# Performance work log

Measured on AMD Instinct MI355X. Metric: run time of the kernel, lower is better.

Reference implementation:

```python
import jax, jax.numpy as jnp
import numpy as np

KB = 0.0019872041      # Boltzmann constant, kcal/(mol*K)
TEMP = 300.0
ALPHA = 10.0
BW = 0.15              # Gaussian KDE bandwidth
PAIR_I = jnp.array([0, 0, 0, 1, 1, 2])
PAIR_J = jnp.array([1, 2, 3, 2, 3, 3])

B, N_ATOMS = 512, 1024
G, L, K, D = 256, 8, 128, 6


def setup_inputs() -> dict:
    key = jax.random.key(0)
    k1, k2, k3, k4, k5, k6 = jax.random.split(key, 6)
    positions = jax.random.normal(k1, (B, N_ATOMS, 3), dtype=jnp.float32) * 2.0
    # KDE training samples live in 6-dim distance space (positive, few Angstroms)
    kde_samples = jax.random.uniform(k2, (G, L, K, D), dtype=jnp.float32) * 5.0
    weight = jax.random.uniform(k3, (G, L), dtype=jnp.float32)
    offset = jax.random.normal(k4, (G, L), dtype=jnp.float32)
    atom_idxs = jax.random.randint(k5, (G, L, 4), 0, N_ATOMS)
    group_sizes = jax.random.randint(k6, (G,), 0, L)  # clamped to >=1 in reference
    return {"positions": positions, "kde_samples": kde_samples, "weight": weight,
            "offset": offset, "atom_idxs": atom_idxs, "group_sizes": group_sizes}


def reference(positions, kde_samples, weight, offset, atom_idxs, group_sizes):
    Gn, Ln, Kn, Dn = kde_samples.shape
    # Gather the 4 vertices of every loss: [B, G, L, 4, 3]
    vp = positions[:, atom_idxs]
    # 6 pairwise distances per loss: [B, G, L, 6]
    diff = vp[..., PAIR_I, :] - vp[..., PAIR_J, :]
    dists = jnp.sqrt(jnp.sum(diff * diff, axis=-1) + 1e-12)
    # Gaussian KDE log-density over the K training samples, expanded squared
    x2 = jnp.sum(dists * dists, axis=-1)          # [B,G,L]
    mu2 = jnp.sum(kde_samples * kde_samples, -1)  # [G,L,K]
    xmu = jnp.einsum('bgld,glkd->bglk', dists, kde_samples)
    sq = x2[..., None] + mu2[None] - 2.0 * xmu    # [B,G,L,K]
    log_norm = jnp.log(jnp.float32(Kn)) + 0.5 * Dn * jnp.log(2.0 * jnp.pi * BW * BW)
    logP = jax.nn.logsumexp(-sq / (2.0 * BW * BW), axis=-1) - log_norm  # [B,G,L]
    energy = -KB * TEMP * logP
    scaled = energy * weight + offset             # [B,G,L]
    # Ragged group reduction: min over the valid losses of each group
    sizes = jnp.maximum(group_sizes, 1)
    mask = jnp.arange(Ln)[None, :] < sizes[:, None]        # [G,L]
    group_min = jnp.min(jnp.where(mask, scaled, jnp.inf), axis=-1)  # [B,G]
    # soft-min across groups
    return -jax.nn.logsumexp(-ALPHA * group_min, axis=-1) / ALPHA   # [B]
```

## Files before the change

kernel.cpp:

```cpp
#include <hip/hip_runtime.h>

#define NB 512
#define NATOMS 1024
#define NG 256
#define NL 8
#define NK 128

#define KBT 0.59616123f
#define ALPHA_C 10.0f
#define LN2 0.6931471805599453f
#define LOG2E 1.4426950408889634f
#define INV2BW2 22.222221f
#define SCALE2 (INV2BW2 * LOG2E)
#define LOG_NORM (-1.0170649f)

#define WL_CAP 2048
#define FILL_BLOCKS 128

typedef _Float16 f16x8 __attribute__((ext_vector_type(8)));
typedef float f32x16 __attribute__((ext_vector_type(16)));

__device__ __forceinline__ float fexp2(float x) { return __builtin_amdgcn_exp2f(x); }
__device__ __forceinline__ float flog2(float x) { return __builtin_amdgcn_logf(x); }

__device__ __forceinline__ unsigned fkey(float f) {
  unsigned u = __float_as_uint(f);
  return (u & 0x80000000u) ? ~u : (u | 0x80000000u);
}
__device__ __forceinline__ float funkey(unsigned k) {
  unsigned u = (k & 0x80000000u) ? (k ^ 0x80000000u) : ~k;
  return __uint_as_float(u);
}

__device__ __forceinline__ float wred_min(float v) {
#pragma unroll
  for (int m = 32; m >= 1; m >>= 1) v = fminf(v, __shfl_xor(v, m, 64));
  return v;
}
__device__ __forceinline__ float wred_sum(float v) {
#pragma unroll
  for (int m = 32; m >= 1; m >>= 1) v += __shfl_xor(v, m, 64);
  return v;
}

__global__ __launch_bounds__(256) void prep_small(
    const int* __restrict__ gsizes, int* __restrict__ wl,
    uint4* __restrict__ gmin_u4) {
  const int t = threadIdx.x;
  if (blockIdx.x != 0) {
    const unsigned F = 0xFFFFFFFFu;
    gmin_u4[(blockIdx.x - 1) * 256 + t] = make_uint4(F, F, F, F);
    return;
  }
  const int lane = t & 63, wid = t >> 6;
  int gs = gsizes[t];
  int nl = gs < 1 ? 1 : (gs > NL ? NL : gs);
  int x = nl;
#pragma unroll
  for (int m = 1; m < 64; m <<= 1) {
    int y = __shfl_up(x, m, 64);
    if (lane >= m) x += y;
  }
  __shared__ int wsum[4];
  if (lane == 63) wsum[wid] = x;
  __syncthreads();
  int off = 0;
  for (int i = 0; i < wid; ++i) off += wsum[i];
  int inc = off + x, exc = inc - nl;
  for (int j = 0; j < nl; ++j) wl[exc + j] = (t << 3) | j;
  if (t == 255) wl[WL_CAP] = inc;
}

__global__ __launch_bounds__(256) void stage1_kernel(
    const float* __restrict__ positions, const float* __restrict__ kde,
    const float* __restrict__ weight, const float* __restrict__ offs,
    const int* __restrict__ atom_idxs, const int* __restrict__ wl,
    unsigned* __restrict__ gmin_u) {
  const int count = wl[WL_CAP];
  const int w = blockIdx.x >> 2;
  if (w >= count) return;
  const int gl = wl[w];
  const int g = gl >> 3;

  const int t = threadIdx.x;
  const int lane = t & 63;
  const int col = lane & 31, h = lane >> 5;
  const int b = ((blockIdx.x & 3) << 7) + ((t >> 6) << 5) + col;

  __shared__ f16x8 tabL[8][64];

  const int4 idx = *reinterpret_cast<const int4*>(atom_idxs + (gl << 2));
  const int ids[4] = {idx.x, idx.y, idx.z, idx.w};
  const float* pb = positions + (size_t)b * NATOMS * 3;
  float ax[4], ay[4], az[4];
#pragma unroll
  for (int j = 0; j < 4; ++j) {
    const float3 p = *reinterpret_cast<const float3*>(pb + ids[j] * 3);
    ax[j] = p.x; ay[j] = p.y; az[j] = p.z;
  }

  if (t < NK) {
    const float* mp = kde + ((size_t)gl * NK + t) * 6;
    float mu2 = 0.0f;
    _Float16 ah[6], al[6];
#pragma unroll
    for (int q = 0; q < 6; ++q) {
      float mv = mp[q];
      mu2 += mv * mv;
      float a = (2.0f * SCALE2) * mv;
      _Float16 hh = (_Float16)a;
      ah[q] = hh;
      al[q] = (_Float16)(a - (float)hh);
    }
    float z = -SCALE2 * mu2;
    _Float16 z1 = (_Float16)z;
    _Float16 z2 = (_Float16)(z - (float)z1);
    const _Float16 Z = (_Float16)0.0f;
    const int kt = t >> 5, m = t & 31;
    tabL[kt * 2 + 0][m]      = (f16x8){ah[0],ah[1],ah[2],ah[3],ah[4],ah[5],al[0],al[1]};
    tabL[kt * 2 + 0][m + 32] = (f16x8){al[2],al[3],al[4],al[5],ah[0],ah[1],ah[2],ah[3]};
    tabL[kt * 2 + 1][m]      = (f16x8){ah[4],ah[5],al[0],al[1],al[2],al[3],al[4],al[5]};
    tabL[kt * 2 + 1][m + 32] = (f16x8){z1,  z2,  Z,   Z,   Z,   Z,   Z,   Z   };
  }

  const int PI_[6] = {0, 0, 0, 1, 1, 2};
  const int PJ_[6] = {1, 2, 3, 2, 3, 3};
  float d[6]; float x2 = 0.0f;
#pragma unroll
  for (int q = 0; q < 6; ++q) {
    float dx = ax[PI_[q]] - ax[PJ_[q]];
    float dy = ay[PI_[q]] - ay[PJ_[q]];
    float dz = az[PI_[q]] - az[PJ_[q]];
    float dd = dx * dx + dy * dy + dz * dz + 1e-12f;
    d[q] = sqrtf(dd);
    x2 += d[q] * d[q];
  }
  const float c2 = -x2 * SCALE2;

  _Float16 xh[6], xl[6];
#pragma unroll
  for (int q = 0; q < 6; ++q) {
    _Float16 hh = (_Float16)d[q];
    xh[q] = hh;
    xl[q] = (_Float16)(d[q] - (float)hh);
  }
  const _Float16 ONE = (_Float16)1.0f, Z = (_Float16)0.0f;
  f16x8 Bf0 = (h == 0)
    ? (f16x8){xh[0],xh[1],xh[2],xh[3],xh[4],xh[5],xh[0],xh[1]}
    : (f16x8){xh[2],xh[3],xh[4],xh[5],xl[0],xl[1],xl[2],xl[3]};
  f16x8 Bf1 = (h == 0)
    ? (f16x8){xl[4],xl[5],xl[0],xl[1],xl[2],xl[3],xl[4],xl[5]}
    : (f16x8){ONE,  ONE,  Z,   Z,   Z,   Z,   Z,   Z   };

  __syncthreads();

  const f32x16 zz = {0.0f};
  f32x16 acc[4];
#pragma unroll
  for (int kt = 0; kt < 4; ++kt) {
    f16x8 A0 = tabL[kt * 2 + 0][lane];
    f16x8 A1 = tabL[kt * 2 + 1][lane];
    acc[kt] = __builtin_amdgcn_mfma_f32_32x32x16_f16(
        A1, Bf1, __builtin_amdgcn_mfma_f32_32x32x16_f16(A0, Bf0, zz, 0, 0, 0),
        0, 0, 0);
  }

  float mkt[4];
#pragma unroll
  for (int kt = 0; kt < 4; ++kt) {
    float m0 = fmaxf(fmaxf(acc[kt][0], acc[kt][1]), fmaxf(acc[kt][2], acc[kt][3]));
    float m1 = fmaxf(fmaxf(acc[kt][4], acc[kt][5]), fmaxf(acc[kt][6], acc[kt][7]));
    float m2 = fmaxf(fmaxf(acc[kt][8], acc[kt][9]), fmaxf(acc[kt][10], acc[kt][11]));
    float m3 = fmaxf(fmaxf(acc[kt][12], acc[kt][13]), fmaxf(acc[kt][14], acc[kt][15]));
    mkt[kt] = fmaxf(fmaxf(m0, m1), fmaxf(m2, m3));
  }
  float mx = fmaxf(fmaxf(mkt[0], mkt[1]), fmaxf(mkt[2], mkt[3]));
  mx = fmaxf(mx, __shfl_xor(mx, 32, 64));

  float s0 = 0.0f, s1 = 0.0f, s2 = 0.0f, s3 = 0.0f;
#pragma unroll
  for (int kt = 0; kt < 4; ++kt) {
    s0 += fexp2(acc[kt][0] - mx)  + fexp2(acc[kt][1] - mx)
        + fexp2(acc[kt][2] - mx)  + fexp2(acc[kt][3] - mx);
    s1 += fexp2(acc[kt][4] - mx)  + fexp2(acc[kt][5] - mx)
        + fexp2(acc[kt][6] - mx)  + fexp2(acc[kt][7] - mx);
    s2 += fexp2(acc[kt][8] - mx)  + fexp2(acc[kt][9] - mx)
        + fexp2(acc[kt][10] - mx) + fexp2(acc[kt][11] - mx);
    s3 += fexp2(acc[kt][12] - mx) + fexp2(acc[kt][13] - mx)
        + fexp2(acc[kt][14] - mx) + fexp2(acc[kt][15] - mx);
  }
  float s = (s0 + s1) + (s2 + s3);
  s += __shfl_xor(s, 32, 64);

  if (h == 0) {
    float lse2 = c2 + mx + flog2(s);
    float logP = lse2 * LN2 - LOG_NORM;
    float scaled = -KBT * logP * weight[gl] + offs[gl];
    atomicMin(&gmin_u[g * NB + b], fkey(scaled));
  }
}

__global__ __launch_bounds__(256) void stage2_kernel(
    const unsigned* __restrict__ gmin_u, float* __restrict__ out) {
  const int b = blockIdx.x;
  const int t = threadIdx.x;
  const int lane = t & 63;
  const int wid = t >> 6;
  float v = funkey(gmin_u[t * NB + b]);
  __shared__ float sm[4], ss[4];
  float m = wred_min(v);
  if (lane == 0) sm[wid] = m;
  __syncthreads();
  float M = fminf(fminf(sm[0], sm[1]), fminf(sm[2], sm[3]));
  float e = fexp2(-ALPHA_C * LOG2E * (v - M));
  float s = wred_sum(e);
  if (lane == 0) ss[wid] = s;
  __syncthreads();
  if (t == 0) {
    float S = ss[0] + ss[1] + ss[2] + ss[3];
    out[b] = M - flog2(S) * LN2 / ALPHA_C;
  }
}

extern "C" void kernel_launch(void* const* d_in, const int* in_sizes, int n_in,
                              void* d_out, int out_size, void* d_ws, size_t ws_size,
                              hipStream_t stream) {
  const float* positions = (const float*)d_in[0];
  const float* kde       = (const float*)d_in[1];
  const float* weight    = (const float*)d_in[2];
  const float* offs      = (const float*)d_in[3];
  const int*   atom_idxs = (const int*)d_in[4];
  const int*   gsizes    = (const int*)d_in[5];
  float* out = (float*)d_out;

  unsigned* gmin_u = (unsigned*)d_ws;
  int* wl = (int*)d_ws + (size_t)NG * NB;

  prep_small<<<dim3(1 + FILL_BLOCKS), dim3(256), 0, stream>>>(
      gsizes, wl, (uint4*)gmin_u);
  stage1_kernel<<<dim3(WL_CAP * 4), dim3(256), 0, stream>>>(
      positions, kde, weight, offs, atom_idxs, wl, gmin_u);
  stage2_kernel<<<dim3(NB), dim3(256), 0, stream>>>(gmin_u, out);
}
```

Before: 35.85 us.

## Transpose positions to atom-major layout for coalesced gathers in stage1

Adds transpose blocks to the prep kernel that rewrite positions from [B, atoms, 3] into an [atom*3, B] layout in workspace through a shared-memory tile. Stage1 then reads each atom coordinate with consecutive batch indices across lanes, which gives coalesced loads in place of strided 12-byte gathers. The cost is a full read and write of the positions array (about 6 MB each way) in the prep kernel on every call, plus extra workspace.

```diff
diff --git a/kernel.cpp b/kernel.cpp
--- a/kernel.cpp
+++ b/kernel.cpp
@@ -16,6 +16,7 @@
 
 #define WL_CAP 2048
 #define FILL_BLOCKS 128
+#define TR_BLOCKS 256
 
 typedef _Float16 f16x8 __attribute__((ext_vector_type(8)));
 typedef float f32x16 __attribute__((ext_vector_type(16)));
@@ -44,35 +45,67 @@
 }
 
 __global__ __launch_bounds__(256) void prep_small(
-    const int* __restrict__ gsizes, int* __restrict__ wl,
-    uint4* __restrict__ gmin_u4) {
+    const float* __restrict__ positions, const int* __restrict__ gsizes,
+    int* __restrict__ wl, uint4* __restrict__ gmin_u4,
+    float* __restrict__ pT) {
   const int t = threadIdx.x;
-  if (blockIdx.x != 0) {
+  const int bid = blockIdx.x;
+  __shared__ int wsum[4];
+  __shared__ float tile[64][97];
+
+  if (bid == 0) {
+    const int lane = t & 63, wid = t >> 6;
+    int gs = gsizes[t];
+    int nl = gs < 1 ? 1 : (gs > NL ? NL : gs);
+    int x = nl;
+#pragma unroll
+    for (int m = 1; m < 64; m <<= 1) {
+      int y = __shfl_up(x, m, 64);
+      if (lane >= m) x += y;
+    }
+    if (lane == 63) wsum[wid] = x;
+    __syncthreads();
+    int off = 0;
+    for (int i = 0; i < wid; ++i) off += wsum[i];
+    int inc = off + x, exc = inc - nl;
+    for (int j = 0; j < nl; ++j) wl[exc + j] = (t << 3) | j;
+    if (t == 255) wl[WL_CAP] = inc;
+    return;
+  }
+  if (bid <= FILL_BLOCKS) {
     const unsigned F = 0xFFFFFFFFu;
-    gmin_u4[(blockIdx.x - 1) * 256 + t] = make_uint4(F, F, F, F);
+    gmin_u4[(bid - 1) * 256 + t] = make_uint4(F, F, F, F);
     return;
   }
-  const int lane = t & 63, wid = t >> 6;
-  int gs = gsizes[t];
-  int nl = gs < 1 ? 1 : (gs > NL ? NL : gs);
-  int x = nl;
-#pragma unroll
-  for (int m = 1; m < 64; m <<= 1) {
-    int y = __shfl_up(x, m, 64);
-    if (lane >= m) x += y;
-  }
-  __shared__ int wsum[4];
-  if (lane == 63) wsum[wid] = x;
-  __syncthreads();
-  int off = 0;
-  for (int i = 0; i < wid; ++i) off += wsum[i];
-  int inc = off + x, exc = inc - nl;
-  for (int j = 0; j < nl; ++j) wl[exc + j] = (t << 3) | j;
-  if (t == 255) wl[WL_CAP] = inc;
+
+  const int tb = bid - (FILL_BLOCKS + 1);
+  const int a0 = (tb >> 3) << 5;
+  const int b0 = (tb & 7) << 6;
+#pragma unroll
+  for (int iter = 0; iter < 6; ++iter) {
+    const int fi = iter * 256 + t;
+    const int i = fi / 24, s = fi - i * 24;
+    const float4 v = *reinterpret_cast<const float4*>(
+        positions + ((size_t)(b0 + i) * NATOMS + a0) * 3 + s * 4);
+    tile[i][s * 4 + 0] = v.x;
+    tile[i][s * 4 + 1] = v.y;
+    tile[i][s * 4 + 2] = v.z;
+    tile[i][s * 4 + 3] = v.w;
+  }
+  __syncthreads();
+  if (t < 96) {
+    float* dst = pT + ((size_t)a0 * 3 + t) * NB + b0;
+#pragma unroll
+    for (int f = 0; f < 16; ++f) {
+      float4 v = make_float4(tile[4 * f + 0][t], tile[4 * f + 1][t],
+                             tile[4 * f + 2][t], tile[4 * f + 3][t]);
+      *reinterpret_cast<float4*>(dst + 4 * f) = v;
+    }
+  }
 }
 
 __global__ __launch_bounds__(256) void stage1_kernel(
-    const float* __restrict__ positions, const float* __restrict__ kde,
+    const float* __restrict__ pT, const float* __restrict__ kde,
     const float* __restrict__ weight, const float* __restrict__ offs,
     const int* __restrict__ atom_idxs, const int* __restrict__ wl,
     unsigned* __restrict__ gmin_u) {
@@ -91,12 +124,13 @@
 
   const int4 idx = *reinterpret_cast<const int4*>(atom_idxs + (gl << 2));
   const int ids[4] = {idx.x, idx.y, idx.z, idx.w};
-  const float* pb = positions + (size_t)b * NATOMS * 3;
   float ax[4], ay[4], az[4];
 #pragma unroll
   for (int j = 0; j < 4; ++j) {
-    const float3 p = *reinterpret_cast<const float3*>(pb + ids[j] * 3);
-    ax[j] = p.x; ay[j] = p.y; az[j] = p.z;
+    const float* pr = pT + (size_t)ids[j] * 3 * NB + b;
+    ax[j] = pr[0];
+    ay[j] = pr[NB];
+    az[j] = pr[2 * NB];
   }
 
   if (t < NK) {
@@ -235,10 +269,11 @@
 
   unsigned* gmin_u = (unsigned*)d_ws;
   int* wl = (int*)d_ws + (size_t)NG * NB;
-
-  prep_small<<<dim3(1 + FILL_BLOCKS), dim3(256), 0, stream>>>(
-      gsizes, wl, (uint4*)gmin_u);
+  float* pT = (float*)((char*)d_ws + (1 << 20));
+
+  prep_small<<<dim3(1 + FILL_BLOCKS + TR_BLOCKS), dim3(256), 0, stream>>>(
+      positions, gsizes, wl, (uint4*)gmin_u, pT);
   stage1_kernel<<<dim3(WL_CAP * 4), dim3(256), 0, stream>>>(
-      positions, kde, weight, offs, atom_idxs, wl, gmin_u);
+      pT, kde, weight, offs, atom_idxs, wl, gmin_u);
   stage2_kernel<<<dim3(NB), dim3(256), 0, stream>>>(gmin_u, out);
 }
```

After: 38.40 us. 1.07x slower.

## Process all batch chunks per block with double-buffered position prefetch

Applied to the files above, without the earlier changes.

Each stage1 block now handles all four 128-wide batch chunks for one loss instead of one chunk. The KDE table is built in shared memory once and reused four times, which removes three quarters of the table setup and block launches. Position gathers for the next chunk are issued before computing the current one, so their latency overlaps the MFMA and exp work. In exchange there are 4x fewer blocks, which lowers parallelism, and register pressure rises from the double buffer.

```diff
diff --git a/kernel.cpp b/kernel.cpp
--- a/kernel.cpp
+++ b/kernel.cpp
@@ -77,26 +77,30 @@
     const int* __restrict__ atom_idxs, const int* __restrict__ wl,
     unsigned* __restrict__ gmin_u) {
   const int count = wl[WL_CAP];
-  const int w = blockIdx.x >> 2;
+  const int w = blockIdx.x;
   if (w >= count) return;
   const int gl = wl[w];
   const int g = gl >> 3;
 
   const int t = threadIdx.x;
   const int lane = t & 63;
+  const int wid = t >> 6;
   const int col = lane & 31, h = lane >> 5;
-  const int b = ((blockIdx.x & 3) << 7) + ((t >> 6) << 5) + col;
 
   __shared__ f16x8 tabL[8][64];
 
   const int4 idx = *reinterpret_cast<const int4*>(atom_idxs + (gl << 2));
   const int ids[4] = {idx.x, idx.y, idx.z, idx.w};
-  const float* pb = positions + (size_t)b * NATOMS * 3;
-  float ax[4], ay[4], az[4];
-#pragma unroll
-  for (int j = 0; j < 4; ++j) {
-    const float3 p = *reinterpret_cast<const float3*>(pb + ids[j] * 3);
-    ax[j] = p.x; ay[j] = p.y; az[j] = p.z;
+
+  float px[2][4], py[2][4], pz[2][4];
+  {
+    const int b = (wid << 5) + col;
+    const float* pb = positions + (size_t)b * NATOMS * 3;
+#pragma unroll
+    for (int j = 0; j < 4; ++j) {
+      const float3 p = *reinterpret_cast<const float3*>(pb + ids[j] * 3);
+      px[0][j] = p.x; py[0][j] = p.y; pz[0][j] = p.z;
+    }
   }
 
   if (t < NK) {
@@ -122,81 +126,97 @@
     tabL[kt * 2 + 1][m]      = (f16x8){ah[4],ah[5],al[0],al[1],al[2],al[3],al[4],al[5]};
     tabL[kt * 2 + 1][m + 32] = (f16x8){z1,  z2,  Z,   Z,   Z,   Z,   Z,   Z   };
   }
-
+  __syncthreads();
+
+  const float wgt = weight[gl], off = offs[gl];
   const int PI_[6] = {0, 0, 0, 1, 1, 2};
   const int PJ_[6] = {1, 2, 3, 2, 3, 3};
-  float d[6]; float x2 = 0.0f;
-#pragma unroll
-  for (int q = 0; q < 6; ++q) {
-    float dx = ax[PI_[q]] - ax[PJ_[q]];
-    float dy = ay[PI_[q]] - ay[PJ_[q]];
-    float dz = az[PI_[q]] - az[PJ_[q]];
-    float dd = dx * dx + dy * dy + dz * dz + 1e-12f;
-    d[q] = sqrtf(dd);
-    x2 += d[q] * d[q];
-  }
-  const float c2 = -x2 * SCALE2;
-
-  _Float16 xh[6], xl[6];
-#pragma unroll
-  for (int q = 0; q < 6; ++q) {
-    _Float16 hh = (_Float16)d[q];
-    xh[q] = hh;
-    xl[q] = (_Float16)(d[q] - (float)hh);
-  }
   const _Float16 ONE = (_Float16)1.0f, Z = (_Float16)0.0f;
-  f16x8 Bf0 = (h == 0)
-    ? (f16x8){xh[0],xh[1],xh[2],xh[3],xh[4],xh[5],xh[0],xh[1]}
-    : (f16x8){xh[2],xh[3],xh[4],xh[5],xl[0],xl[1],xl[2],xl[3]};
-  f16x8 Bf1 = (h == 0)
-    ? (f16x8){xl[4],xl[5],xl[0],xl[1],xl[2],xl[3],xl[4],xl[5]}
-    : (f16x8){ONE,  ONE,  Z,   Z,   Z,   Z,   Z,   Z   };
-
-  __syncthreads();
-
   const f32x16 zz = {0.0f};
-  f32x16 acc[4];
-#pragma unroll
-  for (int kt = 0; kt < 4; ++kt) {
-    f16x8 A0 = tabL[kt * 2 + 0][lane];
-    f16x8 A1 = tabL[kt * 2 + 1][lane];
-    acc[kt] = __builtin_amdgcn_mfma_f32_32x32x16_f16(
-        A1, Bf1, __builtin_amdgcn_mfma_f32_32x32x16_f16(A0, Bf0, zz, 0, 0, 0),
-        0, 0, 0);
-  }
-
-  float mkt[4];
-#pragma unroll
-  for (int kt = 0; kt < 4; ++kt) {
-    float m0 = fmaxf(fmaxf(acc[kt][0], acc[kt][1]), fmaxf(acc[kt][2], acc[kt][3]));
-    float m1 = fmaxf(fmaxf(acc[kt][4], acc[kt][5]), fmaxf(acc[kt][6], acc[kt][7]));
-    float m2 = fmaxf(fmaxf(acc[kt][8], acc[kt][9]), fmaxf(acc[kt][10], acc[kt][11]));
-    float m3 = fmaxf(fmaxf(acc[kt][12], acc[kt][13]), fmaxf(acc[kt][14], acc[kt][15]));
-    mkt[kt] = fmaxf(fmaxf(m0, m1), fmaxf(m2, m3));
-  }
-  float mx = fmaxf(fmaxf(mkt[0], mkt[1]), fmaxf(mkt[2], mkt[3]));
-  mx = fmaxf(mx, __shfl_xor(mx, 32, 64));
-
-  float s0 = 0.0f, s1 = 0.0f, s2 = 0.0f, s3 = 0.0f;
-#pragma unroll
-  for (int kt = 0; kt < 4; ++kt) {
-    s0 += fexp2(acc[kt][0] - mx)  + fexp2(acc[kt][1] - mx)
-        + fexp2(acc[kt][2] - mx)  + fexp2(acc[kt][3] - mx);
-    s1 += fexp2(acc[kt][4] - mx)  + fexp2(acc[kt][5] - mx)
-        + fexp2(acc[kt][6] - mx)  + fexp2(acc[kt][7] - mx);
-    s2 += fexp2(acc[kt][8] - mx)  + fexp2(acc[kt][9] - mx)
-        + fexp2(acc[kt][10] - mx) + fexp2(acc[kt][11] - mx);
-    s3 += fexp2(acc[kt][12] - mx) + fexp2(acc[kt][13] - mx)
-        + fexp2(acc[kt][14] - mx) + fexp2(acc[kt][15] - mx);
-  }
-  float s = (s0 + s1) + (s2 + s3);
-  s += __shfl_xor(s, 32, 64);
-
-  if (h == 0) {
-    float lse2 = c2 + mx + flog2(s);
-    float logP = lse2 * LN2 - LOG_NORM;
-    float scaled = -KBT * logP * weight[gl] + offs[gl];
-    atomicMin(&gmin_u[g * NB + b], fkey(scaled));
+
+#pragma unroll
+  for (int gg = 0; gg < 4; ++gg) {
+    const int cur = gg & 1;
+    if (gg < 3) {
+      const int bn = ((gg + 1) << 7) + (wid << 5) + col;
+      const float* pb = positions + (size_t)bn * NATOMS * 3;
+#pragma unroll
+      for (int j = 0; j < 4; ++j) {
+        const float3 p = *reinterpret_cast<const float3*>(pb + ids[j] * 3);
+        px[cur ^ 1][j] = p.x; py[cur ^ 1][j] = p.y; pz[cur ^ 1][j] = p.z;
+      }
+    }
+    const int b = (gg << 7) + (wid << 5) + col;
+
+    float d[6]; float x2 = 0.0f;
+#pragma unroll
+    for (int q = 0; q < 6; ++q) {
+      float dx = px[cur][PI_[q]] - px[cur][PJ_[q]];
+      float dy = py[cur][PI_[q]] - py[cur][PJ_[q]];
+      float dz = pz[cur][PI_[q]] - pz[cur][PJ_[q]];
+      float dd = dx * dx + dy * dy + dz * dz + 1e-12f;
+      d[q] = sqrtf(dd);
+      x2 += d[q] * d[q];
+    }
+    const float c2 = -x2 * SCALE2;
+
+    _Float16 xh[6], xl[6];
+#pragma unroll
+    for (int q = 0; q < 6; ++q) {
+      _Float16 hh = (_Float16)d[q];
+      xh[q] = hh;
+      xl[q] = (_Float16)(d[q] - (float)hh);
+    }
+    f16x8 Bf0 = (h == 0)
+      ? (f16x8){xh[0],xh[1],xh[2],xh[3],xh[4],xh[5],xh[0],xh[1]}
+      : (f16x8){xh[2],xh[3],xh[4],xh[5],xl[0],xl[1],xl[2],xl[3]};
+    f16x8 Bf1 = (h == 0)
+      ? (f16x8){xl[4],xl[5],xl[0],xl[1],xl[2],xl[3],xl[4],xl[5]}
+      : (f16x8){ONE,  ONE,  Z,   Z,   Z,   Z,   Z,   Z   };
+
+    f32x16 acc[4];
+#pragma unroll
+    for (int kt = 0; kt < 4; ++kt) {
+      f16x8 A0 = tabL[kt * 2 + 0][lane];
+      f16x8 A1 = tabL[kt * 2 + 1][lane];
+      acc[kt] = __builtin_amdgcn_mfma_f32_32x32x16_f16(
+          A1, Bf1, __builtin_amdgcn_mfma_f32_32x32x16_f16(A0, Bf0, zz, 0, 0, 0),
+          0, 0, 0);
+    }
+
+    float mkt[4];
+#pragma unroll
+    for (int kt = 0; kt < 4; ++kt) {
+      float m0 = fmaxf(fmaxf(acc[kt][0], acc[kt][1]), fmaxf(acc[kt][2], acc[kt][3]));
+      float m1 = fmaxf(fmaxf(acc[kt][4], acc[kt][5]), fmaxf(acc[kt][6], acc[kt][7]));
+      float m2 = fmaxf(fmaxf(acc[kt][8], acc[kt][9]), fmaxf(acc[kt][10], acc[kt][11]));
+      float m3 = fmaxf(fmaxf(acc[kt][12], acc[kt][13]), fmaxf(acc[kt][14], acc[kt][15]));
+      mkt[kt] = fmaxf(fmaxf(m0, m1), fmaxf(m2, m3));
+    }
+    float mx = fmaxf(fmaxf(mkt[0], mkt[1]), fmaxf(mkt[2], mkt[3]));
+    mx = fmaxf(mx, __shfl_xor(mx, 32, 64));
+
+    float s0 = 0.0f, s1 = 0.0f, s2 = 0.0f, s3 = 0.0f;
+#pragma unroll
+    for (int kt = 0; kt < 4; ++kt) {
+      s0 += fexp2(acc[kt][0] - mx)  + fexp2(acc[kt][1] - mx)
+          + fexp2(acc[kt][2] - mx)  + fexp2(acc[kt][3] - mx);
+      s1 += fexp2(acc[kt][4] - mx)  + fexp2(acc[kt][5] - mx)
+          + fexp2(acc[kt][6] - mx)  + fexp2(acc[kt][7] - mx);
+      s2 += fexp2(acc[kt][8] - mx)  + fexp2(acc[kt][9] - mx)
+          + fexp2(acc[kt][10] - mx) + fexp2(acc[kt][11] - mx);
+      s3 += fexp2(acc[kt][12] - mx) + fexp2(acc[kt][13] - mx)
+          + fexp2(acc[kt][14] - mx) + fexp2(acc[kt][15] - mx);
+    }
+    float s = (s0 + s1) + (s2 + s3);
+    s += __shfl_xor(s, 32, 64);
+
+    if (h == 0) {
+      float lse2 = c2 + mx + flog2(s);
+      float logP = lse2 * LN2 - LOG_NORM;
+      float scaled = -KBT * logP * wgt + off;
+      atomicMin(&gmin_u[g * NB + b], fkey(scaled));
+    }
   }
 }
 
@@ -238,7 +258,7 @@
 
   prep_small<<<dim3(1 + FILL_BLOCKS), dim3(256), 0, stream>>>(
       gsizes, wl, (uint4*)gmin_u);
-  stage1_kernel<<<dim3(WL_CAP * 4), dim3(256), 0, stream>>>(
+  stage1_kernel<<<dim3(WL_CAP), dim3(256), 0, stream>>>(
       positions, kde, weight, offs, atom_idxs, wl, gmin_u);
   stage2_kernel<<<dim3(NB), dim3(256), 0, stream>>>(gmin_u, out);
 }
```

New measurement: 37.73 us. 5.3% more time.

## Drop prep kernel and atomics; store per-loss values and reduce ragged min in stage2

Applied to the files above, without the earlier changes.

Removes the prep kernel that built a compacted worklist and initialised the atomic-min buffer. Stage1 now launches blocks for every (g,l) pair and exits early for invalid losses; it writes each scaled energy to a plain buffer instead of doing an atomicMin. Stage2 then takes the min over each group's valid losses itself. The MFMA logsumexp is also split into two passes with an online max/sum merge, which lowers the number of live accumulator registers. The cost is a kernel launch and atomics saved, in exchange for more empty blocks, a larger intermediate buffer and strided reads in stage2.

```diff
diff --git a/kernel.cpp b/kernel.cpp
--- a/kernel.cpp
+++ b/kernel.cpp
@@ -14,24 +14,12 @@
 #define SCALE2 (INV2BW2 * LOG2E)
 #define LOG_NORM (-1.0170649f)
 
-#define WL_CAP 2048
-#define FILL_BLOCKS 128
-
 typedef _Float16 f16x8 __attribute__((ext_vector_type(8)));
 typedef float f32x16 __attribute__((ext_vector_type(16)));
 
 __device__ __forceinline__ float fexp2(float x) { return __builtin_amdgcn_exp2f(x); }
 __device__ __forceinline__ float flog2(float x) { return __builtin_amdgcn_logf(x); }
 
-__device__ __forceinline__ unsigned fkey(float f) {
-  unsigned u = __float_as_uint(f);
-  return (u & 0x80000000u) ? ~u : (u | 0x80000000u);
-}
-__device__ __forceinline__ float funkey(unsigned k) {
-  unsigned u = (k & 0x80000000u) ? (k ^ 0x80000000u) : ~k;
-  return __uint_as_float(u);
-}
-
 __device__ __forceinline__ float wred_min(float v) {
 #pragma unroll
   for (int m = 32; m >= 1; m >>= 1) v = fminf(v, __shfl_xor(v, m, 64));
@@ -41,51 +29,24 @@
 #pragma unroll
   for (int m = 32; m >= 1; m >>= 1) v += __shfl_xor(v, m, 64);
   return v;
-}
-
-__global__ __launch_bounds__(256) void prep_small(
-    const int* __restrict__ gsizes, int* __restrict__ wl,
-    uint4* __restrict__ gmin_u4) {
-  const int t = threadIdx.x;
-  if (blockIdx.x != 0) {
-    const unsigned F = 0xFFFFFFFFu;
-    gmin_u4[(blockIdx.x - 1) * 256 + t] = make_uint4(F, F, F, F);
-    return;
-  }
-  const int lane = t & 63, wid = t >> 6;
-  int gs = gsizes[t];
-  int nl = gs < 1 ? 1 : (gs > NL ? NL : gs);
-  int x = nl;
-#pragma unroll
-  for (int m = 1; m < 64; m <<= 1) {
-    int y = __shfl_up(x, m, 64);
-    if (lane >= m) x += y;
-  }
-  __shared__ int wsum[4];
-  if (lane == 63) wsum[wid] = x;
-  __syncthreads();
-  int off = 0;
-  for (int i = 0; i < wid; ++i) off += wsum[i];
-  int inc = off + x, exc = inc - nl;
-  for (int j = 0; j < nl; ++j) wl[exc + j] = (t << 3) | j;
-  if (t == 255) wl[WL_CAP] = inc;
 }
 
 __global__ __launch_bounds__(256) void stage1_kernel(
     const float* __restrict__ positions, const float* __restrict__ kde,
     const float* __restrict__ weight, const float* __restrict__ offs,
-    const int* __restrict__ atom_idxs, const int* __restrict__ wl,
-    unsigned* __restrict__ gmin_u) {
-  const int count = wl[WL_CAP];
-  const int w = blockIdx.x >> 2;
-  if (w >= count) return;
-  const int gl = wl[w];
-  const int g = gl >> 3;
+    const int* __restrict__ atom_idxs, const int* __restrict__ gsizes,
+    float* __restrict__ scaled_out) {
+  const int gl = blockIdx.x >> 2;
+  const int g = gl >> 3, l = gl & 7;
+  int gs = gsizes[g];
+  int nl = gs < 1 ? 1 : (gs > NL ? NL : gs);
+  if (l >= nl) return;
 
   const int t = threadIdx.x;
   const int lane = t & 63;
+  const int wid = t >> 6;
   const int col = lane & 31, h = lane >> 5;
-  const int b = ((blockIdx.x & 3) << 7) + ((t >> 6) << 5) + col;
+  const int b = ((blockIdx.x & 3) << 7) + (wid << 5) + col;
 
   __shared__ f16x8 tabL[8][64];
 
@@ -154,59 +115,72 @@
 
   __syncthreads();
 
-  const f32x16 zz = {0.0f};
-  f32x16 acc[4];
-#pragma unroll
-  for (int kt = 0; kt < 4; ++kt) {
-    f16x8 A0 = tabL[kt * 2 + 0][lane];
-    f16x8 A1 = tabL[kt * 2 + 1][lane];
-    acc[kt] = __builtin_amdgcn_mfma_f32_32x32x16_f16(
-        A1, Bf1, __builtin_amdgcn_mfma_f32_32x32x16_f16(A0, Bf0, zz, 0, 0, 0),
-        0, 0, 0);
-  }
-
-  float mkt[4];
-#pragma unroll
-  for (int kt = 0; kt < 4; ++kt) {
-    float m0 = fmaxf(fmaxf(acc[kt][0], acc[kt][1]), fmaxf(acc[kt][2], acc[kt][3]));
-    float m1 = fmaxf(fmaxf(acc[kt][4], acc[kt][5]), fmaxf(acc[kt][6], acc[kt][7]));
-    float m2 = fmaxf(fmaxf(acc[kt][8], acc[kt][9]), fmaxf(acc[kt][10], acc[kt][11]));
-    float m3 = fmaxf(fmaxf(acc[kt][12], acc[kt][13]), fmaxf(acc[kt][14], acc[kt][15]));
-    mkt[kt] = fmaxf(fmaxf(m0, m1), fmaxf(m2, m3));
-  }
-  float mx = fmaxf(fmaxf(mkt[0], mkt[1]), fmaxf(mkt[2], mkt[3]));
-  mx = fmaxf(mx, __shfl_xor(mx, 32, 64));
-
-  float s0 = 0.0f, s1 = 0.0f, s2 = 0.0f, s3 = 0.0f;
-#pragma unroll
-  for (int kt = 0; kt < 4; ++kt) {
-    s0 += fexp2(acc[kt][0] - mx)  + fexp2(acc[kt][1] - mx)
-        + fexp2(acc[kt][2] - mx)  + fexp2(acc[kt][3] - mx);
-    s1 += fexp2(acc[kt][4] - mx)  + fexp2(acc[kt][5] - mx)
-        + fexp2(acc[kt][6] - mx)  + fexp2(acc[kt][7] - mx);
-    s2 += fexp2(acc[kt][8] - mx)  + fexp2(acc[kt][9] - mx)
-        + fexp2(acc[kt][10] - mx) + fexp2(acc[kt][11] - mx);
-    s3 += fexp2(acc[kt][12] - mx) + fexp2(acc[kt][13] - mx)
-        + fexp2(acc[kt][14] - mx) + fexp2(acc[kt][15] - mx);
-  }
-  float s = (s0 + s1) + (s2 + s3);
-  s += __shfl_xor(s, 32, 64);
+  float mloc = -1e30f, sloc = 0.0f;
+#pragma unroll
+  for (int pass = 0; pass < 2; ++pass) {
+    const f32x16 zz = {0.0f};
+    f32x16 a0, a1;
+    {
+      const int kt = pass * 2;
+      f16x8 A0 = tabL[kt * 2 + 0][lane];
+      f16x8 A1 = tabL[kt * 2 + 1][lane];
+      a0 = __builtin_amdgcn_mfma_f32_32x32x16_f16(
+          A1, Bf1, __builtin_amdgcn_mfma_f32_32x32x16_f16(A0, Bf0, zz, 0, 0, 0),
+          0, 0, 0);
+    }
+    {
+      const int kt = pass * 2 + 1;
+      f16x8 A0 = tabL[kt * 2 + 0][lane];
+      f16x8 A1 = tabL[kt * 2 + 1][lane];
+      a1 = __builtin_amdgcn_mfma_f32_32x32x16_f16(
+          A1, Bf1, __builtin_amdgcn_mfma_f32_32x32x16_f16(A0, Bf0, zz, 0, 0, 0),
+          0, 0, 0);
+    }
+    float m0 = fmaxf(fmaxf(a0[0], a0[1]), fmaxf(a0[2], a0[3]));
+    float m1 = fmaxf(fmaxf(a0[4], a0[5]), fmaxf(a0[6], a0[7]));
+    float m2 = fmaxf(fmaxf(a0[8], a0[9]), fmaxf(a0[10], a0[11]));
+    float m3 = fmaxf(fmaxf(a0[12], a0[13]), fmaxf(a0[14], a0[15]));
+    float m4 = fmaxf(fmaxf(a1[0], a1[1]), fmaxf(a1[2], a1[3]));
+    float m5 = fmaxf(fmaxf(a1[4], a1[5]), fmaxf(a1[6], a1[7]));
+    float m6 = fmaxf(fmaxf(a1[8], a1[9]), fmaxf(a1[10], a1[11]));
+    float m7 = fmaxf(fmaxf(a1[12], a1[13]), fmaxf(a1[14], a1[15]));
+    float mp = fmaxf(fmaxf(fmaxf(m0, m1), fmaxf(m2, m3)),
+                     fmaxf(fmaxf(m4, m5), fmaxf(m6, m7)));
+    float s0 = 0.0f, s1 = 0.0f;
+#pragma unroll
+    for (int i = 0; i < 16; ++i) { s0 += fexp2(a0[i] - mp); s1 += fexp2(a1[i] - mp); }
+    float sp = s0 + s1;
+    float nm = fmaxf(mloc, mp);
+    sloc = fmaf(sloc, fexp2(mloc - nm), sp * fexp2(mp - nm));
+    mloc = nm;
+  }
+
+  float mo = __shfl_xor(mloc, 32, 64);
+  float so = __shfl_xor(sloc, 32, 64);
+  float M = fmaxf(mloc, mo);
+  float S = sloc * fexp2(mloc - M) + so * fexp2(mo - M);
 
   if (h == 0) {
-    float lse2 = c2 + mx + flog2(s);
+    float lse2 = c2 + M + flog2(S);
     float logP = lse2 * LN2 - LOG_NORM;
-    float scaled = -KBT * logP * weight[gl] + offs[gl];
-    atomicMin(&gmin_u[g * NB + b], fkey(scaled));
+    float sc = -KBT * logP * weight[gl] + offs[gl];
+    scaled_out[(size_t)gl * NB + b] = sc;
   }
 }
 
 __global__ __launch_bounds__(256) void stage2_kernel(
-    const unsigned* __restrict__ gmin_u, float* __restrict__ out) {
+    const float* __restrict__ scaled_in, const int* __restrict__ gsizes,
+    float* __restrict__ out) {
   const int b = blockIdx.x;
   const int t = threadIdx.x;
   const int lane = t & 63;
   const int wid = t >> 6;
-  float v = funkey(gmin_u[t * NB + b]);
+  int gs = gsizes[t];
+  int nl = gs < 1 ? 1 : (gs > NL ? NL : gs);
+  float v = 1e30f;
+  for (int l = 0; l < nl; ++l)
+    v = fminf(v, scaled_in[(size_t)((t << 3) + l) * NB + b]);
+
   __shared__ float sm[4], ss[4];
   float m = wred_min(v);
   if (lane == 0) sm[wid] = m;
@@ -233,12 +207,9 @@
   const int*   gsizes    = (const int*)d_in[5];
   float* out = (float*)d_out;
 
-  unsigned* gmin_u = (unsigned*)d_ws;
-  int* wl = (int*)d_ws + (size_t)NG * NB;
-
-  prep_small<<<dim3(1 + FILL_BLOCKS), dim3(256), 0, stream>>>(
-      gsizes, wl, (uint4*)gmin_u);
-  stage1_kernel<<<dim3(WL_CAP * 4), dim3(256), 0, stream>>>(
-      positions, kde, weight, offs, atom_idxs, wl, gmin_u);
-  stage2_kernel<<<dim3(NB), dim3(256), 0, stream>>>(gmin_u, out);
-}
+  float* scaled = (float*)d_ws;
+
+  stage1_kernel<<<dim3(NG * NL * 4), dim3(256), 0, stream>>>(
+      positions, kde, weight, offs, atom_idxs, gsizes, scaled);
+  stage2_kernel<<<dim3(NB), dim3(256), 0, stream>>>(scaled, gsizes, out);
+}
```

Result: slower. 48.34 us (+34.9%).
